# Kernel optimization log

Measured on AMD Instinct MI355X. Metric: run time of the kernel, lower is better.

Reference implementation:

```python
import jax, jax.numpy as jnp
import numpy as np

B, S, P = 16, 1024, 1024
D, H, HD = 128, 8, 16      # embed_dim, num_heads, head_dim (qkv_dim)
MS = 32                    # ms_hidden_dim
E = 524288                 # number of edges
TANH_CLIP = 10.0
TEMP = 1.0
EPS = 1e-9


def setup_inputs() -> dict:
    key = jax.random.key(0)
    ks = jax.random.split(key, 12)
    inv = lambda n: 1.0 / np.sqrt(n)
    return {
        "x1": jax.random.normal(ks[0], (B, S, D), jnp.float32),
        "x2": jax.random.normal(ks[1], (B, P, D), jnp.float32),
        "b_idx": jax.random.randint(ks[2], (E,), 0, B, jnp.int32),
        "s_idx": jax.random.randint(ks[3], (E,), 0, S, jnp.int32),
        "p_idx": jax.random.randint(ks[4], (E,), 0, P, jnp.int32),
        "w": jax.random.uniform(ks[5], (E,), jnp.float32),
        "Wqv1": jax.random.normal(ks[6], (D, 2 * D), jnp.float32) * inv(D),
        "Wkv2": jax.random.normal(ks[7], (D, 2 * D), jnp.float32) * inv(D),
        "Wo1": jax.random.normal(ks[8], (D, D), jnp.float32) * inv(D),
        "Wo2": jax.random.normal(ks[9], (D, D), jnp.float32) * inv(D),
        "msW1": jax.random.normal(ks[10], (H, 2, MS), jnp.float32) * inv(2),
        "msb1": jnp.zeros((H, MS), jnp.float32),
        "msW2": jax.random.normal(ks[11], (H, MS, 1), jnp.float32) * inv(MS),
        "msb2": jnp.zeros((H, 1), jnp.float32),
    }


def _mixed_scores(logits, w, msW1, msb1, msW2, msb2):
    # logits: [E, H], w: [E] -> per-head 2->MS->1 MLP (MatNet MixedScoreFF)
    mixed = jnp.stack([logits, jnp.broadcast_to(w[:, None], logits.shape)], axis=-1)  # [E,H,2]
    hid = jax.nn.relu(jnp.einsum('ehi,him->ehm', mixed, msW1) + msb1)  # [E,H,MS]
    out = (jnp.einsum('ehm,hmo->eho', hid, msW2) + msb2)[..., 0]       # [E,H]
    return TANH_CLIP * jnp.tanh(out) / TEMP


def _group_softmax_combine(logits, values, gid, num_groups):
    # logits: [E,H], values: [E,H,HD]; exp -> segment-sum denom -> weighted scatter
    el = jnp.exp(logits)
    denom = jax.ops.segment_sum(el, gid, num_segments=num_groups)      # [G,H]
    attn = el / (denom[gid] + EPS)                                      # [E,H]
    return jax.ops.segment_sum(attn[:, :, None] * values, gid, num_segments=num_groups)  # [G,H,HD]


def reference(x1, x2, b_idx, s_idx, p_idx, w, Wqv1, Wkv2, Wo1, Wo2, msW1, msb1, msW2, msb2):
    qv1 = (x1 @ Wqv1).reshape(B, S, 2, H, HD)   # [B,S,2,H,HD]
    kv2 = (x2 @ Wkv2).reshape(B, P, 2, H, HD)
    row_flat = b_idx * S + s_idx                # [E]
    col_flat = b_idx * P + p_idx
    qv1_e = qv1.reshape(B * S, 2, H, HD)[row_flat]   # [E,2,H,HD]
    kv2_e = kv2.reshape(B * P, 2, H, HD)[col_flat]
    q, v1 = qv1_e[:, 0], qv1_e[:, 1]
    k, v2 = kv2_e[:, 0], kv2_e[:, 1]
    logits = jnp.einsum('ehd,ehd->eh', q, k) / np.sqrt(HD).astype(np.float32)
    logits = _mixed_scores(logits, w, msW1, msb1, msW2, msb2)
    row_heads = _group_softmax_combine(logits, v2, row_flat, B * S)  # [B*S,H,HD]
    col_heads = _group_softmax_combine(logits, v1, col_flat, B * P)  # [B*P,H,HD]
    h1 = row_heads.reshape(B, S, H * HD) @ Wo1
    h2 = col_heads.reshape(B, P, H * HD) @ Wo2
    return h1, h2
```

## Files before the change

kernel.cpp:

```cpp
#include <hip/hip_runtime.h>
#include <hip/hip_fp16.h>
#include <math.h>

#define BB   16
#define SS   1024
#define PP   1024
#define HH   8
#define MSS  32
#define EE   524288
#define NROW (BB*SS)
#define NCOL (BB*PP)
#define ESTRIDE 5
#define NRWB 512
#define NB   128
#define CHUNK 4096
#define GCAP 96

__device__ __forceinline__ void gemm_tile_core(
        const float* __restrict__ Arow, const float* __restrict__ Bsrc,
        int ldb, int c0, float* As , float* Bs ,
        float4 acc4[8], int t) {
    int tx = t & 31, ty = t >> 5;
#pragma unroll
    for (int li = 0; li < 8; li++) {
        int idx = li * 256 + t;
        int r = idx >> 5, p = idx & 31;
        *(float4*)&As[r * 132 + 4 * p] = *(const float4*)(Arow + r * 128 + 4 * p);
    }
#pragma unroll
    for (int i = 0; i < 8; i++) acc4[i] = make_float4(0.f, 0.f, 0.f, 0.f);

    for (int kc = 0; kc < 4; kc++) {
        __syncthreads();
#pragma unroll
        for (int li = 0; li < 4; li++) {
            int idx = li * 256 + t;
            int kk = idx >> 5, p = idx & 31;
            *(float4*)&Bs[kk * 128 + 4 * p] =
                *(const float4*)(Bsrc + (size_t)(kc * 32 + kk) * ldb + c0 + 4 * p);
        }
        __syncthreads();
#pragma unroll
        for (int kq = 0; kq < 8; kq++) {
            float4 a4[8];
#pragma unroll
            for (int i = 0; i < 8; i++)
                a4[i] = *(const float4*)&As[(ty + 8 * i) * 132 + kc * 32 + kq * 4];
#pragma unroll
            for (int kk = 0; kk < 4; kk++) {
                float4 b4 = *(const float4*)&Bs[(kq * 4 + kk) * 128 + 4 * tx];
#pragma unroll
                for (int i = 0; i < 8; i++) {
                    float av = ((const float*)&a4[i])[kk];
                    acc4[i].x = fmaf(av, b4.x, acc4[i].x);
                    acc4[i].y = fmaf(av, b4.y, acc4[i].y);
                    acc4[i].z = fmaf(av, b4.z, acc4[i].z);
                    acc4[i].w = fmaf(av, b4.w, acc4[i].w);
                }
            }
        }
    }
}

__global__ __launch_bounds__(256, 2) void proj_kernel(
        const float* __restrict__ x1, const float* __restrict__ x2,
        const float* __restrict__ Wqv1, const float* __restrict__ Wkv2,
        float* __restrict__ qf, float* __restrict__ kf,
        __half* __restrict__ v1h, __half* __restrict__ v2h) {
    __shared__ float As[64 * 132];
    __shared__ float Bs[32 * 256];
    int t = threadIdx.x;
    int bid = blockIdx.x;
    int matrix = bid >> 8;
    int mb = bid & 255;
    const float* A  = matrix ? x2 : x1;
    const float* Bm = matrix ? Wkv2 : Wqv1;
    const float* Arow = A + (size_t)mb * 64 * 128;

    int tx = t & 31, ty = t >> 5;
#pragma unroll
    for (int li = 0; li < 8; li++) {
        int idx = li * 256 + t;
        int r = idx >> 5, p = idx & 31;
        *(float4*)&As[r * 132 + 4 * p] = *(const float4*)(Arow + r * 128 + 4 * p);
    }
    float4 accL[8], accR[8];
#pragma unroll
    for (int i = 0; i < 8; i++) {
        accL[i] = make_float4(0.f, 0.f, 0.f, 0.f);
        accR[i] = make_float4(0.f, 0.f, 0.f, 0.f);
    }

    for (int kc = 0; kc < 4; kc++) {
        __syncthreads();
#pragma unroll
        for (int li = 0; li < 8; li++) {
            int idx = li * 256 + t;
            int kk = idx >> 6, p = idx & 63;
            *(float4*)&Bs[kk * 256 + 4 * p] =
                *(const float4*)(Bm + (size_t)(kc * 32 + kk) * 256 + 4 * p);
        }
        __syncthreads();
#pragma unroll
        for (int kq = 0; kq < 8; kq++) {
            float4 a4[8];
#pragma unroll
            for (int i = 0; i < 8; i++)
                a4[i] = *(const float4*)&As[(ty + 8 * i) * 132 + kc * 32 + kq * 4];
#pragma unroll
            for (int kk = 0; kk < 4; kk++) {
                float4 bL = *(const float4*)&Bs[(kq * 4 + kk) * 256 + 4 * tx];
                float4 bR = *(const float4*)&Bs[(kq * 4 + kk) * 256 + 128 + 4 * tx];
#pragma unroll
                for (int i = 0; i < 8; i++) {
                    float av = ((const float*)&a4[i])[kk];
                    accL[i].x = fmaf(av, bL.x, accL[i].x);
                    accL[i].y = fmaf(av, bL.y, accL[i].y);
                    accL[i].z = fmaf(av, bL.z, accL[i].z);
                    accL[i].w = fmaf(av, bL.w, accL[i].w);
                    accR[i].x = fmaf(av, bR.x, accR[i].x);
                    accR[i].y = fmaf(av, bR.y, accR[i].y);
                    accR[i].z = fmaf(av, bR.z, accR[i].z);
                    accR[i].w = fmaf(av, bR.w, accR[i].w);
                }
            }
        }
    }

    float* Cq = matrix ? kf : qf;
    __half* Cv = matrix ? v2h : v1h;
#pragma unroll
    for (int i = 0; i < 8; i++) {
        int row = mb * 64 + ty + 8 * i;
        *(float4*)(Cq + (size_t)row * 128 + 4 * tx) = accL[i];
        __half2* p = (__half2*)(Cv + (size_t)row * 128 + 4 * tx);
        p[0] = __halves2half2(__float2half(accR[i].x), __float2half(accR[i].y));
        p[1] = __halves2half2(__float2half(accR[i].z), __float2half(accR[i].w));
    }
}

__global__ __launch_bounds__(256) void outp_kernel(
        const float* __restrict__ rh, const float* __restrict__ ch,
        const float* __restrict__ Wo1, const float* __restrict__ Wo2,
        float* __restrict__ out) {
    __shared__ float As[64 * 132];
    __shared__ float Bs[32 * 128];
    int t = threadIdx.x;
    int matrix = blockIdx.x >> 8;
    int mb = blockIdx.x & 255;
    const float* A  = matrix ? ch : rh;
    const float* Bm = matrix ? Wo2 : Wo1;
    float* C = out + (size_t)matrix * NROW * 128;

    float4 acc4[8];
    gemm_tile_core(A + (size_t)mb * 64 * 128, Bm, 128, 0, As, Bs, acc4, t);

    int tx = t & 31, ty = t >> 5;
#pragma unroll
    for (int i = 0; i < 8; i++) {
        int row = mb * 64 + ty + 8 * i;
        *(float4*)(C + (size_t)row * 128 + 4 * tx) = acc4[i];
    }
}

__global__ __launch_bounds__(1024) void hist_kernel(
        const int* __restrict__ b_idx, const int* __restrict__ s_idx,
        const int* __restrict__ p_idx, unsigned int* __restrict__ ph) {
    __shared__ unsigned int lh[16384];
    int t = threadIdx.x;
#pragma unroll
    for (int i = 0; i < 16; i++) lh[t + 1024 * i] = 0;
    __syncthreads();
    int base = blockIdx.x * CHUNK;
#pragma unroll
    for (int k = 0; k < 4; k++) {
        int e = base + k * 1024 + t;
        int b = b_idx[e];
        int rbin = (b << 10) + s_idx[e];
        int cbin = 16384 + (b << 10) + p_idx[e];
        atomicAdd(&lh[rbin >> 1], 1u << (16 * (rbin & 1)));
        atomicAdd(&lh[cbin >> 1], 1u << (16 * (cbin & 1)));
    }
    __syncthreads();
    unsigned int* dst = ph + (size_t)blockIdx.x * 16384;
#pragma unroll
    for (int i = 0; i < 16; i++) dst[t + 1024 * i] = lh[t + 1024 * i];
}

__global__ __launch_bounds__(128) void scan1_kernel(
        const unsigned int* __restrict__ ph, int* __restrict__ pbase,
        int* __restrict__ tot) {
    int bin = blockIdx.x * 128 + threadIdx.x;
    int word = bin >> 1;
    int sh = 16 * (bin & 1);
    int run = 0;
#pragma unroll 8
    for (int j = 0; j < NB; j++) {
        unsigned int v = ph[(size_t)j * 16384 + word];
        pbase[(size_t)j * 32768 + bin] = run;
        run += (v >> sh) & 0xffff;
    }
    tot[bin] = run;
}

__global__ __launch_bounds__(1024) void scan2_kernel(
        const int* __restrict__ tot, int* __restrict__ offs) {
    __shared__ int sdata[1024];
    int side = blockIdx.x;
    int t = threadIdx.x;
    const int* c = tot + side * 16384;
    int* o = offs + side * (16384 + 1);
    int base = t * 16;
    int loc[16];
    int run = 0;
#pragma unroll
    for (int i = 0; i < 16; i++) { loc[i] = run; run += c[base + i]; }
    sdata[t] = run;
    __syncthreads();
    for (int st = 1; st < 1024; st <<= 1) {
        int v = (t >= st) ? sdata[t - st] : 0;
        __syncthreads();
        sdata[t] += v;
        __syncthreads();
    }
    int excl = sdata[t] - run;
#pragma unroll
    for (int i = 0; i < 16; i++) o[base + i] = excl + loc[i];
    if (t == 1023) o[16384] = sdata[1023];
}

__global__ __launch_bounds__(1024) void pos_kernel(
        const int* __restrict__ b_idx, const int* __restrict__ s_idx,
        const int* __restrict__ p_idx, const float* __restrict__ w,
        const int* __restrict__ pbase, const int* __restrict__ offs,
        int4* __restrict__ ebuf) {
    __shared__ int cur[16384];
    int t = threadIdx.x;
    {
        const int* src = pbase + (size_t)blockIdx.x * 32768 + 16384;
        const int* oc = offs + (16384 + 1);
#pragma unroll
        for (int i = 0; i < 16; i++) {
            int idx = t + 1024 * i;
            cur[idx] = oc[idx] + src[idx];
        }
    }
    __syncthreads();
    int base = blockIdx.x * CHUNK;
    int rowr[4], colr[4], pcr[4];
    float wr[4];
#pragma unroll
    for (int k = 0; k < 4; k++) {
        int e = base + k * 1024 + t;
        int b = b_idx[e];
        rowr[k] = (b << 10) + s_idx[e];
        colr[k] = (b << 10) + p_idx[e];
        wr[k] = w[e];
        pcr[k] = atomicAdd(&cur[colr[k]], 1);
    }
    __syncthreads();
    {
        const int* src = pbase + (size_t)blockIdx.x * 32768;
#pragma unroll
        for (int i = 0; i < 16; i++) {
            int idx = t + 1024 * i;
            cur[idx] = offs[idx] + src[idx];
        }
    }
    __syncthreads();
#pragma unroll
    for (int k = 0; k < 4; k++) {
        int pr = atomicAdd(&cur[rowr[k]], 1);
        ebuf[pr] = make_int4(rowr[k], colr[k], __float_as_int(wr[k]), pcr[k]);
    }
}

__global__ __launch_bounds__(256) void edge_kernel(
        const float* __restrict__ qf, const float* __restrict__ kf,
        const int4* __restrict__ ebuf, const int* __restrict__ offs_row,
        const float* __restrict__ msW1, const float* __restrict__ msb1,
        const float* __restrict__ msW2, const float* __restrict__ msb2,
        float* __restrict__ entr, float* __restrict__ entc) {
    __shared__ float4 sPk[8 * 33];
    __shared__ float sB2[8];
    int t = threadIdx.x;
    {
        int h = t >> 5, m = t & 31;
        sPk[h * 33 + m] = make_float4(msW1[h * 64 + m], msW1[h * 64 + 32 + m],
                                      msb1[h * 32 + m], msW2[h * 32 + m]);
    }
    if (t < 8) sB2[t] = msb2[t];
    __syncthreads();

    int x = blockIdx.x & 7;
    int ridx = blockIdx.x >> 3;
    int wv = t >> 6;
    int lane = t & 63;
    int l = lane & 7;
    int g = lane >> 3;

    int rl = ridx * 4 + wv;
    int row = ((x + ((rl >> 10) << 3)) << 10) + (rl & 1023);
    int s = offs_row[row];
    int cnt = offs_row[row + 1] - s;

    int hh = 2 * (l & 3) + (l >> 2);
    const float4* wp = &sPk[hh * 33];
    float bias2 = sB2[hh];

    const float4* qp4 = (const float4*)(qf + (size_t)row * 128);
    float4 q0 = qp4[l], q1 = qp4[8 + l], q2 = qp4[16 + l], q3 = qp4[24 + l];

    for (int j0 = 0; j0 < cnt; j0 += 8) {
        int j = j0 + g;
        if (j < cnt) {
            int pos = s + j;
            int4 rec = ebuf[pos];
            int col = rec.y;
            float we = __int_as_float(rec.z);
            int pc = rec.w;

            const float4* kp4 = (const float4*)(kf + (size_t)col * 128);
            float p0, p1, p2, p3;
            {
                float4 k4 = kp4[l];
                p0 = fmaf(q0.x, k4.x, fmaf(q0.y, k4.y, fmaf(q0.z, k4.z, q0.w * k4.w)));
            }
            {
                float4 k4 = kp4[8 + l];
                p1 = fmaf(q1.x, k4.x, fmaf(q1.y, k4.y, fmaf(q1.z, k4.z, q1.w * k4.w)));
            }
            {
                float4 k4 = kp4[16 + l];
                p2 = fmaf(q2.x, k4.x, fmaf(q2.y, k4.y, fmaf(q2.z, k4.z, q2.w * k4.w)));
            }
            {
                float4 k4 = kp4[24 + l];
                p3 = fmaf(q3.x, k4.x, fmaf(q3.y, k4.y, fmaf(q3.z, k4.z, q3.w * k4.w)));
            }
            p0 += __shfl_xor(p0, 1); p0 += __shfl_xor(p0, 2);
            p1 += __shfl_xor(p1, 1); p1 += __shfl_xor(p1, 2);
            p2 += __shfl_xor(p2, 1); p2 += __shfl_xor(p2, 2);
            p3 += __shfl_xor(p3, 1); p3 += __shfl_xor(p3, 2);

            int js = l & 3;
            float dot = js == 0 ? p0 : (js == 1 ? p1 : (js == 2 ? p2 : p3));
            float logit = dot * 0.25f;

            float outv = bias2;
#pragma unroll 4
            for (int m = 0; m < MSS; m++) {
                float4 c = wp[m];
                float hid = fmaf(logit, c.x, fmaf(we, c.y, c.z));
                hid = fmaxf(hid, 0.f);
                outv = fmaf(hid, c.w, outv);
            }
            float u  = __expf(outv + outv);
            float th = 1.0f - 2.0f * __builtin_amdgcn_rcpf(u + 1.0f);
            float ev = __expf(10.0f * th);
            __half evh = __float2half(ev);

            float* er = entr + (size_t)pos * ESTRIDE;
            float* ec = entc + (size_t)pc * ESTRIDE;
            ((__half*)er)[2 + hh] = evh;
            ((__half*)ec)[2 + hh] = evh;
            if (l == 0) {
                er[0] = __int_as_float(col);
                ec[0] = __int_as_float(row);
            }
        }
    }
}

__global__ __launch_bounds__(128) void combine_kernel(
        const float* __restrict__ entr, const float* __restrict__ entc,
        const int* __restrict__ offs_row, const int* __restrict__ offs_col,
        const __half* __restrict__ v1h, const __half* __restrict__ v2h,
        float* __restrict__ row_heads, float* __restrict__ col_heads) {
    __shared__ float sE[GCAP * ESTRIDE];
    int x = blockIdx.x & 7;
    int r = blockIdx.x >> 3;
    int which = r >> 10;
    int sidx = r & 1023;
    int b = x + ((which & 1) << 3);
    int gl = (b << 10) + sidx;

    int t = threadIdx.x;
    int h = t >> 4;
    const float* ent; const __half* vals; const int* offs; float* outp;
    if (which < 2) { ent = entr; vals = v2h; offs = offs_row; outp = row_heads; }
    else           { ent = entc; vals = v1h; offs = offs_col; outp = col_heads; }
    int s = offs[gl], e_ = offs[gl + 1];
    int cnt = e_ - s;
    int cap = cnt < GCAP ? cnt : GCAP;

    const float* gsrc = ent + (size_t)s * ESTRIDE;
    for (int i = t; i < cap * ESTRIDE; i += 128) sE[i] = gsrc[i];
    __syncthreads();

    float acc = 0.f, den = 0.f;
#pragma unroll 8
    for (int i = 0; i < cap; i++) {
        const float* en = &sE[i * ESTRIDE];
        int other = __float_as_int(en[0]);
        float ev = __half2float(((const __half*)en)[2 + h]);
        float v = __half2float(vals[(size_t)other * 128 + t]);
        acc = fmaf(ev, v, acc);
        den += ev;
    }
    for (int i = cap; i < cnt; i++) {
        const float* en = gsrc + (size_t)i * ESTRIDE;
        int other = __float_as_int(en[0]);
        float ev = __half2float(((const __half*)en)[2 + h]);
        float v = __half2float(vals[(size_t)other * 128 + t]);
        acc = fmaf(ev, v, acc);
        den += ev;
    }
    outp[(size_t)gl * 128 + t] = acc / (den + 1e-9f);
}

extern "C" void kernel_launch(void* const* d_in, const int* in_sizes, int n_in,
                              void* d_out, int out_size, void* d_ws, size_t ws_size,
                              hipStream_t stream) {
    const float* x1   = (const float*)d_in[0];
    const float* x2   = (const float*)d_in[1];
    const int* b_idx  = (const int*)d_in[2];
    const int* s_idx  = (const int*)d_in[3];
    const int* p_idx  = (const int*)d_in[4];
    const float* w    = (const float*)d_in[5];
    const float* Wqv1 = (const float*)d_in[6];
    const float* Wkv2 = (const float*)d_in[7];
    const float* Wo1  = (const float*)d_in[8];
    const float* Wo2  = (const float*)d_in[9];
    const float* msW1 = (const float*)d_in[10];
    const float* msb1 = (const float*)d_in[11];
    const float* msW2 = (const float*)d_in[12];
    const float* msb2 = (const float*)d_in[13];
    float* out = (float*)d_out;

    float* qf = (float*)d_ws;
    float* kf = qf + (size_t)NROW * 128;
    __half* v1h = (__half*)(kf + (size_t)NCOL * 128);
    __half* v2h = v1h + (size_t)NROW * 128;
    float* entr = (float*)(v2h + (size_t)NCOL * 128);
    float* entc = entr + (size_t)EE * ESTRIDE;
    float* row_heads = entc + (size_t)EE * ESTRIDE;
    float* col_heads = row_heads + (size_t)NROW * 128;
    int4* ebuf = (int4*)(col_heads + (size_t)NCOL * 128);
    int* offs = (int*)(ebuf + EE);
    int* tot  = offs + 2 * (16384 + 1);
    unsigned int* ph = (unsigned int*)entc;
    int* pbase = (int*)row_heads;

    hist_kernel<<<NB, 1024, 0, stream>>>(b_idx, s_idx, p_idx, ph);
    scan1_kernel<<<256, 128, 0, stream>>>(ph, pbase, tot);
    scan2_kernel<<<2, 1024, 0, stream>>>(tot, offs);
    pos_kernel<<<NB, 1024, 0, stream>>>(b_idx, s_idx, p_idx, w, pbase, offs, ebuf);

    proj_kernel<<<512, 256, 0, stream>>>(x1, x2, Wqv1, Wkv2, qf, kf, v1h, v2h);

    edge_kernel<<<8 * NRWB, 256, 0, stream>>>(
        qf, kf, ebuf, offs, msW1, msb1, msW2, msb2, entr, entc);

    combine_kernel<<<2 * NROW, 128, 0, stream>>>(
        entr, entc, offs, offs + (16384 + 1), v1h, v2h, row_heads, col_heads);

    outp_kernel<<<512, 256, 0, stream>>>(row_heads, col_heads, Wo1, Wo2, out);
}
```

Measured before the change: 245.7 us.

## Double-buffer weight tiles via direct global-to-LDS loads in projection GEMMs

Both the projection and output GEMM kernels now stage weight tiles in two 16-row LDS buffers filled with global_load_lds, which copies from global memory straight into LDS without passing through registers. The next tile is prefetched while the current one is being used, so each K step needs one barrier instead of two. This is meant to hide global-load latency and cut register traffic in the GEMM stages. The cost is more loop iterations, and correctness depends on the barrier placement and on the asynchronous LDS writes completing in time.

```diff
diff --git a/kernel.cpp b/kernel.cpp
--- a/kernel.cpp
+++ b/kernel.cpp
@@ -16,51 +16,9 @@
 #define CHUNK 4096
 #define GCAP 96
 
-__device__ __forceinline__ void gemm_tile_core(
-        const float* __restrict__ Arow, const float* __restrict__ Bsrc,
-        int ldb, int c0, float* As , float* Bs ,
-        float4 acc4[8], int t) {
-    int tx = t & 31, ty = t >> 5;
-#pragma unroll
-    for (int li = 0; li < 8; li++) {
-        int idx = li * 256 + t;
-        int r = idx >> 5, p = idx & 31;
-        *(float4*)&As[r * 132 + 4 * p] = *(const float4*)(Arow + r * 128 + 4 * p);
-    }
-#pragma unroll
-    for (int i = 0; i < 8; i++) acc4[i] = make_float4(0.f, 0.f, 0.f, 0.f);
-
-    for (int kc = 0; kc < 4; kc++) {
-        __syncthreads();
-#pragma unroll
-        for (int li = 0; li < 4; li++) {
-            int idx = li * 256 + t;
-            int kk = idx >> 5, p = idx & 31;
-            *(float4*)&Bs[kk * 128 + 4 * p] =
-                *(const float4*)(Bsrc + (size_t)(kc * 32 + kk) * ldb + c0 + 4 * p);
-        }
-        __syncthreads();
-#pragma unroll
-        for (int kq = 0; kq < 8; kq++) {
-            float4 a4[8];
-#pragma unroll
-            for (int i = 0; i < 8; i++)
-                a4[i] = *(const float4*)&As[(ty + 8 * i) * 132 + kc * 32 + kq * 4];
-#pragma unroll
-            for (int kk = 0; kk < 4; kk++) {
-                float4 b4 = *(const float4*)&Bs[(kq * 4 + kk) * 128 + 4 * tx];
-#pragma unroll
-                for (int i = 0; i < 8; i++) {
-                    float av = ((const float*)&a4[i])[kk];
-                    acc4[i].x = fmaf(av, b4.x, acc4[i].x);
-                    acc4[i].y = fmaf(av, b4.y, acc4[i].y);
-                    acc4[i].z = fmaf(av, b4.z, acc4[i].z);
-                    acc4[i].w = fmaf(av, b4.w, acc4[i].w);
-                }
-            }
-        }
-    }
-}
+#define GLL(gp, lp) __builtin_amdgcn_global_load_lds( \
+    (const __attribute__((address_space(1))) void*)(gp), \
+    (__attribute__((address_space(3))) void*)(lp), 16, 0, 0)
 
 __global__ __launch_bounds__(256, 2) void proj_kernel(
         const float* __restrict__ x1, const float* __restrict__ x2,
@@ -68,7 +26,7 @@
         float* __restrict__ qf, float* __restrict__ kf,
         __half* __restrict__ v1h, __half* __restrict__ v2h) {
     __shared__ float As[64 * 132];
-    __shared__ float Bs[32 * 256];
+    __shared__ float Bs[2][16 * 256];
     int t = threadIdx.x;
     int bid = blockIdx.x;
     int matrix = bid >> 8;
@@ -84,6 +42,12 @@
         int r = idx >> 5, p = idx & 31;
         *(float4*)&As[r * 132 + 4 * p] = *(const float4*)(Arow + r * 128 + 4 * p);
     }
+#pragma unroll
+    for (int li = 0; li < 4; li++) {
+        int idx = li * 256 + t;
+        GLL(Bm + 4 * idx, &Bs[0][4 * idx]);
+    }
+
     float4 accL[8], accR[8];
 #pragma unroll
     for (int i = 0; i < 8; i++) {
@@ -91,26 +55,29 @@
         accR[i] = make_float4(0.f, 0.f, 0.f, 0.f);
     }
 
-    for (int kc = 0; kc < 4; kc++) {
-        __syncthreads();
-#pragma unroll
-        for (int li = 0; li < 8; li++) {
-            int idx = li * 256 + t;
-            int kk = idx >> 6, p = idx & 63;
-            *(float4*)&Bs[kk * 256 + 4 * p] =
-                *(const float4*)(Bm + (size_t)(kc * 32 + kk) * 256 + 4 * p);
-        }
-        __syncthreads();
-#pragma unroll
-        for (int kq = 0; kq < 8; kq++) {
+    __syncthreads();
+
+    for (int kc = 0; kc < 8; kc++) {
+        if (kc < 7) {
+            const float* src = Bm + (size_t)(kc + 1) * 16 * 256;
+            float* dst = Bs[(kc + 1) & 1];
+#pragma unroll
+            for (int li = 0; li < 4; li++) {
+                int idx = li * 256 + t;
+                GLL(src + 4 * idx, dst + 4 * idx);
+            }
+        }
+        const float* Bcur = Bs[kc & 1];
+#pragma unroll
+        for (int kq = 0; kq < 4; kq++) {
             float4 a4[8];
 #pragma unroll
             for (int i = 0; i < 8; i++)
-                a4[i] = *(const float4*)&As[(ty + 8 * i) * 132 + kc * 32 + kq * 4];
+                a4[i] = *(const float4*)&As[(ty + 8 * i) * 132 + kc * 16 + kq * 4];
 #pragma unroll
             for (int kk = 0; kk < 4; kk++) {
-                float4 bL = *(const float4*)&Bs[(kq * 4 + kk) * 256 + 4 * tx];
-                float4 bR = *(const float4*)&Bs[(kq * 4 + kk) * 256 + 128 + 4 * tx];
+                float4 bL = *(const float4*)&Bcur[(kq * 4 + kk) * 256 + 4 * tx];
+                float4 bR = *(const float4*)&Bcur[(kq * 4 + kk) * 256 + 128 + 4 * tx];
 #pragma unroll
                 for (int i = 0; i < 8; i++) {
                     float av = ((const float*)&a4[i])[kk];
@@ -125,6 +92,7 @@
                 }
             }
         }
+        __syncthreads();
     }
 
     float* Cq = matrix ? kf : qf;
@@ -144,18 +112,67 @@
         const float* __restrict__ Wo1, const float* __restrict__ Wo2,
         float* __restrict__ out) {
     __shared__ float As[64 * 132];
-    __shared__ float Bs[32 * 128];
+    __shared__ float Bs[2][16 * 128];
     int t = threadIdx.x;
     int matrix = blockIdx.x >> 8;
     int mb = blockIdx.x & 255;
     const float* A  = matrix ? ch : rh;
     const float* Bm = matrix ? Wo2 : Wo1;
     float* C = out + (size_t)matrix * NROW * 128;
+    const float* Arow = A + (size_t)mb * 64 * 128;
+
+    int tx = t & 31, ty = t >> 5;
+#pragma unroll
+    for (int li = 0; li < 8; li++) {
+        int idx = li * 256 + t;
+        int r = idx >> 5, p = idx & 31;
+        *(float4*)&As[r * 132 + 4 * p] = *(const float4*)(Arow + r * 128 + 4 * p);
+    }
+#pragma unroll
+    for (int li = 0; li < 2; li++) {
+        int idx = li * 256 + t;
+        GLL(Bm + 4 * idx, &Bs[0][4 * idx]);
+    }
 
     float4 acc4[8];
-    gemm_tile_core(A + (size_t)mb * 64 * 128, Bm, 128, 0, As, Bs, acc4, t);
-
-    int tx = t & 31, ty = t >> 5;
+#pragma unroll
+    for (int i = 0; i < 8; i++) acc4[i] = make_float4(0.f, 0.f, 0.f, 0.f);
+
+    __syncthreads();
+
+    for (int kc = 0; kc < 8; kc++) {
+        if (kc < 7) {
+            const float* src = Bm + (size_t)(kc + 1) * 16 * 128;
+            float* dst = Bs[(kc + 1) & 1];
+#pragma unroll
+            for (int li = 0; li < 2; li++) {
+                int idx = li * 256 + t;
+                GLL(src + 4 * idx, dst + 4 * idx);
+            }
+        }
+        const float* Bcur = Bs[kc & 1];
+#pragma unroll
+        for (int kq = 0; kq < 4; kq++) {
+            float4 a4[8];
+#pragma unroll
+            for (int i = 0; i < 8; i++)
+                a4[i] = *(const float4*)&As[(ty + 8 * i) * 132 + kc * 16 + kq * 4];
+#pragma unroll
+            for (int kk = 0; kk < 4; kk++) {
+                float4 b4 = *(const float4*)&Bcur[(kq * 4 + kk) * 128 + 4 * tx];
+#pragma unroll
+                for (int i = 0; i < 8; i++) {
+                    float av = ((const float*)&a4[i])[kk];
+                    acc4[i].x = fmaf(av, b4.x, acc4[i].x);
+                    acc4[i].y = fmaf(av, b4.y, acc4[i].y);
+                    acc4[i].z = fmaf(av, b4.z, acc4[i].z);
+                    acc4[i].w = fmaf(av, b4.w, acc4[i].w);
+                }
+            }
+        }
+        __syncthreads();
+    }
+
 #pragma unroll
     for (int i = 0; i < 8; i++) {
         int row = mb * 64 + ty + 8 * i;
```

New measurement: 241.9 us (median of 3 runs). No clear change (-1.6%).
